# Kernel tuning notes

Measured on AMD Instinct MI355X. Metric: run time of the kernel, lower is better.

Reference implementation:

```python
import jax, jax.numpy as jnp
import numpy as np

H, D, BS = 32, 128, 16  # num heads, head dim, paged-KV block size
ROPE_BASE = 10000.0
NEG_INF = -1e30


def setup_inputs() -> dict:
    key = jax.random.key(0)
    ks = jax.random.split(key, 8)
    B, KV, hidden = 8, 2048, H * D  # decode: one new token per sequence
    max_blocks = KV // BS
    num_slots = B * KV

    hidden_states = jax.random.normal(ks[0], (B, hidden), jnp.float32) * 0.02

    # rotary cos/sin for the current position of each sequence (pos = KV-1)
    inv_freq = 1.0 / (ROPE_BASE ** (jnp.arange(0, D, 2, dtype=jnp.float32) / D))
    pos = jnp.full((B,), KV - 1, jnp.float32)
    ang = pos[:, None] * inv_freq[None, :]            # [B, D/2]
    cos, sin = jnp.cos(ang), jnp.sin(ang)

    w_qkv = jax.random.normal(ks[1], (3 * H * D, hidden), jnp.float32) * 0.02
    b_qkv = jax.random.normal(ks[2], (3 * H * D,), jnp.float32) * 0.02
    w_o = jax.random.normal(ks[3], (hidden, H * D), jnp.float32) * 0.02

    k_cache = jax.random.normal(ks[4], (num_slots, H, D), jnp.float32) * 0.5
    v_cache = jax.random.normal(ks[5], (num_slots, H, D), jnp.float32) * 0.5

    # contiguous block allocation: seq b owns blocks [b*max_blocks, (b+1)*max_blocks)
    block_tables = jnp.arange(B * max_blocks, dtype=jnp.int32).reshape(B, max_blocks)
    slots = (jnp.arange(B, dtype=jnp.int32) * KV + (KV - 1)).astype(jnp.int32)
    input_lengths = jnp.full((B,), KV, jnp.int32)

    return dict(hidden_states=hidden_states, cos=cos, sin=sin,
                w_qkv=w_qkv, b_qkv=b_qkv, w_o=w_o,
                k_cache=k_cache, v_cache=v_cache,
                block_tables=block_tables, slots=slots,
                input_lengths=input_lengths, max_s=KV)


def _rope(x, cos, sin):
    # flash-attn style (non-interleaved) rotary: split head dim in halves
    x1, x2 = jnp.split(x, 2, axis=-1)                 # [T, H, D/2] each
    c, s = cos[:, None, :], sin[:, None, :]
    return jnp.concatenate([x1 * c - x2 * s, x1 * s + x2 * c], axis=-1)


def reference(hidden_states, cos, sin, w_qkv, b_qkv, w_o,
              k_cache, v_cache, block_tables, slots, input_lengths, max_s):
    B = hidden_states.shape[0]
    # fused QKV projection (c_attn, bias=True)
    qkv = hidden_states @ w_qkv.T + b_qkv             # [B, 3*H*D]
    q, k, v = jnp.split(qkv, 3, axis=1)
    q = q.reshape(B, H, D)
    k = k.reshape(B, H, D)
    v = v.reshape(B, H, D)

    # rotary applied in-place to q and k[:,0] in the original
    q = _rope(q, cos, sin)
    k = _rope(k, cos, sin)

    # reshape_and_cache: scatter current k/v into the paged KV cache
    k_cache = k_cache.at[slots].set(k)
    v_cache = v_cache.at[slots].set(v)

    # paged_attn: gather KV via block tables, masked softmax over valid length
    pos = jnp.arange(max_s)                           # [S]
    idx = block_tables[:, pos // BS] * BS + (pos % BS)[None, :]  # [B, S] slot ids
    keys = k_cache[idx]                               # [B, S, H, D]
    vals = v_cache[idx]                               # [B, S, H, D]

    scale = D ** -0.5
    scores = jnp.einsum('bhd,bshd->bhs', q, keys) * scale
    valid = pos[None, :] < input_lengths[:, None]     # [B, S]
    scores = jnp.where(valid[:, None, :], scores, NEG_INF)
    probs = jax.nn.softmax(scores, axis=-1)
    attn = jnp.einsum('bhs,bshd->bhd', probs, vals)   # [B, H, D]

    # o_proj (c_proj, bias=False)
    return attn.reshape(B, H * D) @ w_o.T
```

## Files before the change

kernel.cpp:

```cpp
#include <hip/hip_runtime.h>

#define NH 32
#define HD 128
#define PBS 16
#define HIDDEN (NH * HD)
#define QKVN (3 * HIDDEN)
#define NSPLIT 8
#define KC 512

template <int NR>
__global__ __launch_bounds__(256) void gemv_lds(const float* __restrict__ x,
                                                const float* __restrict__ W,
                                                const float* __restrict__ bias,
                                                float* __restrict__ out,
                                                int N, int K) {
    __shared__ float xs[8][KC];
    const int tid  = threadIdx.x;
    const int lane = tid & 63;
    const int wid  = tid >> 6;
    const int n0   = blockIdx.x * (NR * 4) + wid * NR;
    const float* w0 = W + (size_t)n0 * K;

    float acc[NR][8];
#pragma unroll
    for (int r = 0; r < NR; ++r)
#pragma unroll
        for (int b = 0; b < 8; ++b) acc[r][b] = 0.f;

    for (int kc = 0; kc < K; kc += KC) {
        __syncthreads();
        {
            const int bq  = tid >> 5;
            const int t32 = tid & 31;
            const float* xb = x + (size_t)bq * K + kc;
#pragma unroll
            for (int j = 0; j < 4; ++j) {
                const int off = (t32 + j * 32) * 4;
                *reinterpret_cast<float4*>(&xs[bq][off]) =
                    *reinterpret_cast<const float4*>(xb + off);
            }
        }
        __syncthreads();
#pragma unroll
        for (int j = 0; j < 2; ++j) {
            const int kk = lane * 4 + j * 256;
            float4 w4[NR];
#pragma unroll
            for (int r = 0; r < NR; ++r)
                w4[r] = *reinterpret_cast<const float4*>(w0 + (size_t)r * K + kc + kk);
#pragma unroll
            for (int b = 0; b < 8; ++b) {
                const float4 x4 = *reinterpret_cast<const float4*>(&xs[b][kk]);
#pragma unroll
                for (int r = 0; r < NR; ++r)
                    acc[r][b] += w4[r].x * x4.x + w4[r].y * x4.y +
                                 w4[r].z * x4.z + w4[r].w * x4.w;
            }
        }
    }
#pragma unroll
    for (int r = 0; r < NR; ++r)
#pragma unroll
        for (int b = 0; b < 8; ++b)
#pragma unroll
            for (int off = 32; off > 0; off >>= 1)
                acc[r][b] += __shfl_xor(acc[r][b], off, 64);
    if (lane == 0) {
#pragma unroll
        for (int r = 0; r < NR; ++r) {
            const float bv = bias ? bias[n0 + r] : 0.f;
#pragma unroll
            for (int b = 0; b < 8; ++b)
                out[(size_t)b * N + n0 + r] = acc[r][b] + bv;
        }
    }
}

__global__ __launch_bounds__(256) void rope_k(float* __restrict__ qkv,
                                              const float* __restrict__ cosb,
                                              const float* __restrict__ sinb,
                                              int B) {
    const int tid = blockIdx.x * blockDim.x + threadIdx.x;
    const int total = 2 * B * NH * (HD / 2);
    if (tid >= total) return;
    const int d = tid % (HD / 2);
    const int h = (tid / (HD / 2)) % NH;
    const int b = (tid / (HD / 2) / NH) % B;
    const int part = tid / (HD / 2) / NH / B;
    const float c = cosb[b * (HD / 2) + d];
    const float s = sinb[b * (HD / 2) + d];
    float* p = qkv + (size_t)b * QKVN + part * HIDDEN + h * HD + d;
    const float x1 = p[0];
    const float x2 = p[HD / 2];
    p[0]      = x1 * c - x2 * s;
    p[HD / 2] = x1 * s + x2 * c;
}

__global__ __launch_bounds__(256) void attn_part(const float* __restrict__ qkv,
                                                 const float* __restrict__ k_cache,
                                                 const float* __restrict__ v_cache,
                                                 const int* __restrict__ block_tables,
                                                 const int* __restrict__ slots,
                                                 const int* __restrict__ lengths,
                                                 float* __restrict__ part_o,
                                                 float* __restrict__ part_ml,
                                                 int S, int max_blocks) {
    const int split = blockIdx.x % NSPLIT;
    const int bh    = blockIdx.x / NSPLIT;
    const int b     = bh >> 5;
    const int h     = bh & 31;
    const int SP    = S / NSPLIT;
    const int base  = split * SP;

    extern __shared__ float smem[];
    float* sc    = smem;
    int*   bt    = (int*)(smem + SP);
    float* red   = smem + SP + SP / PBS;
    float* stage = red + 16;

    const int tid  = threadIdx.x;
    const int lane = tid & 63;
    const int wid  = tid >> 6;
    const int nw   = blockDim.x >> 6;
    const int half = lane >> 5;
    const int l32  = lane & 31;

    const int nbt = SP / PBS;
    for (int i = tid; i < nbt; i += blockDim.x)
        bt[i] = block_tables[b * max_blocks + base / PBS + i];
    __syncthreads();

    const int slot_b = slots[b];
    const int len    = lengths[b];
    const float scale = 0.088388347648318447f;

    const float* qp   = qkv + (size_t)b * QKVN + h * HD;
    const float* newk = qp + HIDDEN;
    const float* newv = qp + 2 * HIDDEN;
    const float4 q4 = *reinterpret_cast<const float4*>(qp + l32 * 4);

    const int STEP = nw * 16;
    for (int s0 = wid * 16; s0 < SP; s0 += STEP) {
        float4 k4[8];
#pragma unroll
        for (int u = 0; u < 8; ++u) {
            const int p = s0 + u * 2 + half;
            const int idx = bt[p >> 4] * PBS + (p & (PBS - 1));
            const float* kp = (idx == slot_b) ? newk
                                              : (k_cache + (size_t)idx * HIDDEN + h * HD);
            k4[u] = *reinterpret_cast<const float4*>(kp + l32 * 4);
        }
#pragma unroll
        for (int u = 0; u < 8; ++u) {
            const int p = s0 + u * 2 + half;
            float d = k4[u].x * q4.x + k4[u].y * q4.y + k4[u].z * q4.z + k4[u].w * q4.w;
#pragma unroll
            for (int off = 16; off > 0; off >>= 1) d += __shfl_xor(d, off, 64);
            if (l32 == 0) sc[p] = (base + p < len) ? d * scale : -1e30f;
        }
    }
    __syncthreads();

    float m = -1e30f;
    for (int s = tid; s < SP; s += blockDim.x) m = fmaxf(m, sc[s]);
#pragma unroll
    for (int off = 32; off > 0; off >>= 1) m = fmaxf(m, __shfl_xor(m, off, 64));
    if (lane == 0) red[wid] = m;
    __syncthreads();
    float bm = red[0];
    for (int w = 1; w < nw; ++w) bm = fmaxf(bm, red[w]);
    __syncthreads();

    float lsum = 0.f;
    for (int s = tid; s < SP; s += blockDim.x) {
        const float e = __expf(sc[s] - bm);
        sc[s] = e;
        lsum += e;
    }
#pragma unroll
    for (int off = 32; off > 0; off >>= 1) lsum += __shfl_xor(lsum, off, 64);
    if (lane == 0) red[wid] = lsum;
    __syncthreads();
    float tot = 0.f;
    for (int w = 0; w < nw; ++w) tot += red[w];

    float4 acc[8];
#pragma unroll
    for (int u = 0; u < 8; ++u) acc[u] = make_float4(0.f, 0.f, 0.f, 0.f);
    for (int s0 = wid * 16; s0 < SP; s0 += STEP) {
        float4 v4[8];
        float pr[8];
#pragma unroll
        for (int u = 0; u < 8; ++u) {
            const int p = s0 + u * 2 + half;
            const int idx = bt[p >> 4] * PBS + (p & (PBS - 1));
            const float* vp = (idx == slot_b) ? newv
                                              : (v_cache + (size_t)idx * HIDDEN + h * HD);
            v4[u] = *reinterpret_cast<const float4*>(vp + l32 * 4);
            pr[u] = sc[p];
        }
#pragma unroll
        for (int u = 0; u < 8; ++u) {
            acc[u].x += pr[u] * v4[u].x;
            acc[u].y += pr[u] * v4[u].y;
            acc[u].z += pr[u] * v4[u].z;
            acc[u].w += pr[u] * v4[u].w;
        }
    }
    float4 a = acc[0];
#pragma unroll
    for (int u = 1; u < 8; ++u) {
        a.x += acc[u].x; a.y += acc[u].y; a.z += acc[u].z; a.w += acc[u].w;
    }
    a.x += __shfl_xor(a.x, 32, 64);
    a.y += __shfl_xor(a.y, 32, 64);
    a.z += __shfl_xor(a.z, 32, 64);
    a.w += __shfl_xor(a.w, 32, 64);

    if (half == 0)
        *reinterpret_cast<float4*>(&stage[wid * HD + l32 * 4]) = a;
    __syncthreads();
    if (wid == 0) {
        float t0 = 0.f, t1 = 0.f;
        for (int w = 0; w < nw; ++w) {
            t0 += stage[w * HD + lane * 2];
            t1 += stage[w * HD + lane * 2 + 1];
        }
        float* po = part_o + ((size_t)bh * NSPLIT + split) * HD;
        po[lane * 2]     = t0;
        po[lane * 2 + 1] = t1;
        if (lane == 0) {
            part_ml[((size_t)bh * NSPLIT + split) * 2]     = bm;
            part_ml[((size_t)bh * NSPLIT + split) * 2 + 1] = tot;
        }
    }
}

__global__ __launch_bounds__(HD) void attn_reduce(const float* __restrict__ part_o,
                                                  const float* __restrict__ part_ml,
                                                  float* __restrict__ attn_out) {
    const int bh = blockIdx.x;
    const int d  = threadIdx.x;
    float M = -1e30f;
#pragma unroll
    for (int i = 0; i < NSPLIT; ++i)
        M = fmaxf(M, part_ml[((size_t)bh * NSPLIT + i) * 2]);
    float L = 0.f, o = 0.f;
#pragma unroll
    for (int i = 0; i < NSPLIT; ++i) {
        const float mi = part_ml[((size_t)bh * NSPLIT + i) * 2];
        const float li = part_ml[((size_t)bh * NSPLIT + i) * 2 + 1];
        const float w  = __expf(mi - M);
        L += li * w;
        o += part_o[((size_t)bh * NSPLIT + i) * HD + d] * w;
    }
    attn_out[(size_t)bh * HD + d] = o / L;
}

extern "C" void kernel_launch(void* const* d_in, const int* in_sizes, int n_in,
                              void* d_out, int out_size, void* d_ws, size_t ws_size,
                              hipStream_t stream) {
    const float* hidden  = (const float*)d_in[0];
    const float* cosb    = (const float*)d_in[1];
    const float* sinb    = (const float*)d_in[2];
    const float* w_qkv   = (const float*)d_in[3];
    const float* b_qkv   = (const float*)d_in[4];
    const float* w_o     = (const float*)d_in[5];
    const float* k_cache = (const float*)d_in[6];
    const float* v_cache = (const float*)d_in[7];
    const int*   btab    = (const int*)d_in[8];
    const int*   slots   = (const int*)d_in[9];
    const int*   lens    = (const int*)d_in[10];

    const int B = in_sizes[0] / HIDDEN;
    const int max_blocks = in_sizes[8] / B;
    const int S = max_blocks * PBS;

    float* qkv     = (float*)d_ws;
    float* attn    = qkv + (size_t)B * QKVN;
    float* part_o  = attn + (size_t)B * HIDDEN;
    float* part_ml = part_o + (size_t)B * NH * NSPLIT * HD;
    float* out     = (float*)d_out;

    gemv_lds<4><<<QKVN / 16, 256, 0, stream>>>(hidden, w_qkv, b_qkv, qkv, QKVN, HIDDEN);

    {
        const int total = 2 * B * NH * (HD / 2);
        rope_k<<<(total + 255) / 256, 256, 0, stream>>>(qkv, cosb, sinb, B);
    }

    {
        const int SP = S / NSPLIT;
        const size_t smem = (size_t)(SP + SP / PBS + 16 + 4 * HD) * sizeof(float);
        attn_part<<<B * NH * NSPLIT, 256, smem, stream>>>(qkv, k_cache, v_cache,
                                                          btab, slots, lens,
                                                          part_o, part_ml, S, max_blocks);
        attn_reduce<<<B * NH, HD, 0, stream>>>(part_o, part_ml, attn);
    }

    gemv_lds<2><<<HIDDEN / 8, 256, 0, stream>>>(attn, w_o, nullptr, out, HIDDEN, HIDDEN);
}
```

Measured before the change: 186.6 us.

## Fuse QK and PV passes into single-pass online softmax in attn_part

Replaces the three-phase split attention (scores to LDS, block max/sum reductions, second pass over V) with a single streaming loop that loads K and V together and keeps a running max, sum and accumulator per half-wave. Partial states are merged across half-waves with shuffles and across waves through a small static LDS stage. This removes the LDS score buffer, several block barriers and the second block-table walk. In exchange it does extra exp and rescale work per chunk, uses more registers with K and V tiles live together, and hardcodes 4 waves and a 64-entry block table in shared memory.

```diff
diff --git a/kernel.cpp b/kernel.cpp
--- a/kernel.cpp
+++ b/kernel.cpp
@@ -112,16 +112,13 @@
     const int SP    = S / NSPLIT;
     const int base  = split * SP;
 
-    extern __shared__ float smem[];
-    float* sc    = smem;
-    int*   bt    = (int*)(smem + SP);
-    float* red   = smem + SP + SP / PBS;
-    float* stage = red + 16;
+    __shared__ int   bt[64];
+    __shared__ float stage[4][HD + 2];
 
     const int tid  = threadIdx.x;
     const int lane = tid & 63;
     const int wid  = tid >> 6;
-    const int nw   = blockDim.x >> 6;
+    const int nw   = 4;
     const int half = lane >> 5;
     const int l32  = lane & 31;
 
@@ -139,9 +136,14 @@
     const float* newv = qp + 2 * HIDDEN;
     const float4 q4 = *reinterpret_cast<const float4*>(qp + l32 * 4);
 
+    float m = -1e30f, l = 0.f;
+    float4 acc[8];
+#pragma unroll
+    for (int u = 0; u < 8; ++u) acc[u] = make_float4(0.f, 0.f, 0.f, 0.f);
+
     const int STEP = nw * 16;
     for (int s0 = wid * 16; s0 < SP; s0 += STEP) {
-        float4 k4[8];
+        float4 k4[8], v4[8];
 #pragma unroll
         for (int u = 0; u < 8; ++u) {
             const int p = s0 + u * 2 + half;
@@ -149,62 +151,38 @@
             const float* kp = (idx == slot_b) ? newk
                                               : (k_cache + (size_t)idx * HIDDEN + h * HD);
             k4[u] = *reinterpret_cast<const float4*>(kp + l32 * 4);
-        }
-#pragma unroll
-        for (int u = 0; u < 8; ++u) {
-            const int p = s0 + u * 2 + half;
-            float d = k4[u].x * q4.x + k4[u].y * q4.y + k4[u].z * q4.z + k4[u].w * q4.w;
-#pragma unroll
-            for (int off = 16; off > 0; off >>= 1) d += __shfl_xor(d, off, 64);
-            if (l32 == 0) sc[p] = (base + p < len) ? d * scale : -1e30f;
-        }
-    }
-    __syncthreads();
-
-    float m = -1e30f;
-    for (int s = tid; s < SP; s += blockDim.x) m = fmaxf(m, sc[s]);
-#pragma unroll
-    for (int off = 32; off > 0; off >>= 1) m = fmaxf(m, __shfl_xor(m, off, 64));
-    if (lane == 0) red[wid] = m;
-    __syncthreads();
-    float bm = red[0];
-    for (int w = 1; w < nw; ++w) bm = fmaxf(bm, red[w]);
-    __syncthreads();
-
-    float lsum = 0.f;
-    for (int s = tid; s < SP; s += blockDim.x) {
-        const float e = __expf(sc[s] - bm);
-        sc[s] = e;
-        lsum += e;
-    }
-#pragma unroll
-    for (int off = 32; off > 0; off >>= 1) lsum += __shfl_xor(lsum, off, 64);
-    if (lane == 0) red[wid] = lsum;
-    __syncthreads();
-    float tot = 0.f;
-    for (int w = 0; w < nw; ++w) tot += red[w];
-
-    float4 acc[8];
-#pragma unroll
-    for (int u = 0; u < 8; ++u) acc[u] = make_float4(0.f, 0.f, 0.f, 0.f);
-    for (int s0 = wid * 16; s0 < SP; s0 += STEP) {
-        float4 v4[8];
-        float pr[8];
-#pragma unroll
-        for (int u = 0; u < 8; ++u) {
-            const int p = s0 + u * 2 + half;
-            const int idx = bt[p >> 4] * PBS + (p & (PBS - 1));
             const float* vp = (idx == slot_b) ? newv
                                               : (v_cache + (size_t)idx * HIDDEN + h * HD);
             v4[u] = *reinterpret_cast<const float4*>(vp + l32 * 4);
-            pr[u] = sc[p];
-        }
-#pragma unroll
-        for (int u = 0; u < 8; ++u) {
-            acc[u].x += pr[u] * v4[u].x;
-            acc[u].y += pr[u] * v4[u].y;
-            acc[u].z += pr[u] * v4[u].z;
-            acc[u].w += pr[u] * v4[u].w;
+        }
+        float sc[8];
+#pragma unroll
+        for (int u = 0; u < 8; ++u) {
+            float d = k4[u].x * q4.x + k4[u].y * q4.y + k4[u].z * q4.z + k4[u].w * q4.w;
+#pragma unroll
+            for (int off = 16; off > 0; off >>= 1) d += __shfl_xor(d, off, 64);
+            const int p = s0 + u * 2 + half;
+            sc[u] = (base + p < len) ? d * scale : -1e30f;
+        }
+        float pm = sc[0];
+#pragma unroll
+        for (int u = 1; u < 8; ++u) pm = fmaxf(pm, sc[u]);
+        const float mn = fmaxf(m, pm);
+        const float r = __expf(m - mn);
+        m = mn;
+        l *= r;
+        float pu[8];
+#pragma unroll
+        for (int u = 0; u < 8; ++u) {
+            pu[u] = __expf(sc[u] - mn);
+            l += pu[u];
+        }
+#pragma unroll
+        for (int u = 0; u < 8; ++u) {
+            acc[u].x = fmaf(pu[u], v4[u].x, acc[u].x * r);
+            acc[u].y = fmaf(pu[u], v4[u].y, acc[u].y * r);
+            acc[u].z = fmaf(pu[u], v4[u].z, acc[u].z * r);
+            acc[u].w = fmaf(pu[u], v4[u].w, acc[u].w * r);
         }
     }
     float4 a = acc[0];
@@ -212,26 +190,47 @@
     for (int u = 1; u < 8; ++u) {
         a.x += acc[u].x; a.y += acc[u].y; a.z += acc[u].z; a.w += acc[u].w;
     }
-    a.x += __shfl_xor(a.x, 32, 64);
-    a.y += __shfl_xor(a.y, 32, 64);
-    a.z += __shfl_xor(a.z, 32, 64);
-    a.w += __shfl_xor(a.w, 32, 64);
-
-    if (half == 0)
-        *reinterpret_cast<float4*>(&stage[wid * HD + l32 * 4]) = a;
+    {
+        const float m2 = __shfl_xor(m, 32, 64);
+        const float l2 = __shfl_xor(l, 32, 64);
+        float4 a2;
+        a2.x = __shfl_xor(a.x, 32, 64);
+        a2.y = __shfl_xor(a.y, 32, 64);
+        a2.z = __shfl_xor(a.z, 32, 64);
+        a2.w = __shfl_xor(a.w, 32, 64);
+        const float M  = fmaxf(m, m2);
+        const float e1 = __expf(m - M);
+        const float e2 = __expf(m2 - M);
+        l = l * e1 + l2 * e2;
+        a.x = a.x * e1 + a2.x * e2;
+        a.y = a.y * e1 + a2.y * e2;
+        a.z = a.z * e1 + a2.z * e2;
+        a.w = a.w * e1 + a2.w * e2;
+        m = M;
+    }
+    if (half == 0) {
+        *reinterpret_cast<float4*>(&stage[wid][l32 * 4]) = a;
+        if (l32 == 0) { stage[wid][HD] = m; stage[wid][HD + 1] = l; }
+    }
     __syncthreads();
     if (wid == 0) {
-        float t0 = 0.f, t1 = 0.f;
-        for (int w = 0; w < nw; ++w) {
-            t0 += stage[w * HD + lane * 2];
-            t1 += stage[w * HD + lane * 2 + 1];
+        float M4 = stage[0][HD];
+#pragma unroll
+        for (int w = 1; w < 4; ++w) M4 = fmaxf(M4, stage[w][HD]);
+        float L = 0.f, t0 = 0.f, t1 = 0.f;
+#pragma unroll
+        for (int w = 0; w < 4; ++w) {
+            const float e = __expf(stage[w][HD] - M4);
+            L  += stage[w][HD + 1] * e;
+            t0 += stage[w][lane * 2] * e;
+            t1 += stage[w][lane * 2 + 1] * e;
         }
         float* po = part_o + ((size_t)bh * NSPLIT + split) * HD;
         po[lane * 2]     = t0;
         po[lane * 2 + 1] = t1;
         if (lane == 0) {
-            part_ml[((size_t)bh * NSPLIT + split) * 2]     = bm;
-            part_ml[((size_t)bh * NSPLIT + split) * 2 + 1] = tot;
+            part_ml[((size_t)bh * NSPLIT + split) * 2]     = M4;
+            part_ml[((size_t)bh * NSPLIT + split) * 2 + 1] = L;
         }
     }
 }
@@ -289,14 +288,10 @@
         rope_k<<<(total + 255) / 256, 256, 0, stream>>>(qkv, cosb, sinb, B);
     }
 
-    {
-        const int SP = S / NSPLIT;
-        const size_t smem = (size_t)(SP + SP / PBS + 16 + 4 * HD) * sizeof(float);
-        attn_part<<<B * NH * NSPLIT, 256, smem, stream>>>(qkv, k_cache, v_cache,
-                                                          btab, slots, lens,
-                                                          part_o, part_ml, S, max_blocks);
-        attn_reduce<<<B * NH, HD, 0, stream>>>(part_o, part_ml, attn);
-    }
+    attn_part<<<B * NH * NSPLIT, 256, 0, stream>>>(qkv, k_cache, v_cache,
+                                                   btab, slots, lens,
+                                                   part_o, part_ml, S, max_blocks);
+    attn_reduce<<<B * NH, HD, 0, stream>>>(part_o, part_ml, attn);
 
     gemv_lds<2><<<HIDDEN / 8, 256, 0, stream>>>(attn, w_o, nullptr, out, HIDDEN, HIDDEN);
 }
```

Result: no change. 184.4 us (-1.2%).
